# Optimization experiments

Measured on AMD Instinct MI355X. Metric: run time of the kernel, lower is better.

Reference implementation:

```python
import jax, jax.numpy as jnp
import numpy as np

ALPHA = 0.2  # LeakyReLU negative slope
NEG_INF = -9e15


def setup_inputs() -> dict:
    key = jax.random.key(0)
    k1, k2, k3, k4 = jax.random.split(key, 4)
    B, N, Fin, Fout = 8, 2048, 512, 256
    x = jax.random.normal(k1, (B, N, Fin), dtype=jnp.float32)
    adj = jax.random.randint(k2, (B, N, N), 0, 2, dtype=jnp.int32)
    # xavier_uniform-like init, gain=1.414
    limW = 1.414 * np.sqrt(6.0 / (Fin + Fout))
    W = jax.random.uniform(k3, (Fin, Fout), jnp.float32, -limW, limW)
    lima = 1.414 * np.sqrt(6.0 / (2 * Fout + 1))
    a = jax.random.uniform(k4, (2 * Fout, 1), jnp.float32, -lima, lima)
    return {"x": x, "adj": adj, "W": W, "a": a}


def reference(x, adj, W, a):
    # x: [B,N,Fin], adj: [B,N,N], W: [Fin,Fout], a: [2*Fout,1]
    Fout = W.shape[1]
    h = jnp.einsum('bnf,fo->bno', x, W)                      # [B,N,Fout]
    a1 = a[:Fout, 0]                                         # source part
    a2 = a[Fout:, 0]                                         # target part
    # e_ij = LeakyReLU(a1.h_i + a2.h_j) -- decomposed, no O(N^2*2F) tensor
    s = h @ a1                                               # [B,N]
    t = h @ a2                                               # [B,N]
    e = jax.nn.leaky_relu(s[:, :, None] + t[:, None, :], ALPHA)  # [B,N,N]
    e = jnp.where(adj > 0, e, NEG_INF)
    attention = jax.nn.softmax(e, axis=2)                    # dropout p=0 (eval)
    h_prime = jnp.einsum('bij,bjo->bio', attention, h)       # [B,N,Fout]
    return jax.nn.elu(h_prime)                               # concat=True -> ELU
```

## Files before the change

### kernel.cpp

```cpp
#include <hip/hip_runtime.h>
#include <hip/hip_bf16.h>

typedef __attribute__((ext_vector_type(8))) short short8;
typedef __attribute__((ext_vector_type(4))) float f32x4;

constexpr int Bb = 8, NN = 2048, FIN = 512, FOUT = 256;
#define LRALPHA 0.2f
#define MFMA16(a, b, c) __builtin_amdgcn_mfma_f32_16x16x32_bf16((a), (b), (c), 0, 0, 0)

static __device__ __forceinline__ ushort f2bf(float f) {
    unsigned u = __float_as_uint(f);
    u += 0x7fffu + ((u >> 16) & 1u);
    return (ushort)(u >> 16);
}
static __device__ __forceinline__ float bf2f(ushort b) { return __uint_as_float(((unsigned)b) << 16); }

#define LDSBAR() do { asm volatile("s_waitcnt lgkmcnt(0)" ::: "memory"); \
                      __builtin_amdgcn_s_barrier(); \
                      asm volatile("" ::: "memory"); } while (0)
#define BARONLY() do { asm volatile("" ::: "memory"); \
                       __builtin_amdgcn_s_barrier(); \
                       asm volatile("" ::: "memory"); } while (0)

__global__ __launch_bounds__(256) void prep(const float* __restrict__ W,
                                            const float* __restrict__ a,
                                            ushort* __restrict__ WTh,
                                            ushort* __restrict__ WTl,
                                            float* __restrict__ wa1,
                                            float* __restrict__ wa2) {
    __shared__ float r1[4], r2[4];
    const int k = blockIdx.x, n = threadIdx.x;
    const int lane = n & 63, wv = n >> 6;
    const float w = W[(size_t)k * FOUT + n];
    const ushort hi = f2bf(w);
    WTh[(size_t)n * FIN + k] = hi;
    WTl[(size_t)n * FIN + k] = f2bf(w - bf2f(hi));
    float p1 = w * a[n], p2 = w * a[FOUT + n];
#pragma unroll
    for (int m = 1; m < 64; m <<= 1) {
        p1 += __shfl_xor(p1, m);
        p2 += __shfl_xor(p2, m);
    }
    if (lane == 0) { r1[wv] = p1; r2[wv] = p2; }
    __syncthreads();
    if (n == 0) {
        wa1[k] = r1[0] + r1[1] + r1[2] + r1[3];
        wa2[k] = r2[0] + r2[1] + r2[2] + r2[3];
    }
}

__global__ __launch_bounds__(512, 2) void gemm_h(const float* __restrict__ x,
                                                 const ushort* __restrict__ WTh,
                                                 const ushort* __restrict__ WTl,
                                                 const float* __restrict__ wa1,
                                                 const float* __restrict__ wa2,
                                                 ushort* __restrict__ hTh,
                                                 float* __restrict__ sv,
                                                 float* __restrict__ tv) {
    __shared__ ushort Ah[4][2][512];
    __shared__ ushort Tr[8][16][72];

    const int t = threadIdx.x, lane = t & 63, w = t >> 6;
    const int m0 = blockIdx.x * 64;

    const int lr = t >> 3, c8 = (t & 7) * 8;
    const int aif = lr >> 4, akstep = c8 >> 5, ak8 = (c8 >> 3) & 3;
    ushort* adst = &Ah[aif][akstep][(((ak8 << 4) | (lr & 15))) * 8];
    const float* xp = x + (size_t)(m0 + lr) * FIN + c8;

    const size_t b0 = (size_t)(w * 32 + (lane & 15)) * FIN + (lane >> 4) * 8;
    const size_t b1 = b0 + (size_t)16 * FIN;
    const ushort *ph0 = WTh + b0, *pl0 = WTl + b0;
    const ushort *ph1 = WTh + b1, *pl1 = WTl + b1;

    f32x4 acc[4][2];
#pragma unroll
    for (int f = 0; f < 4; ++f) {
        acc[f][0] = (f32x4){0.f, 0.f, 0.f, 0.f};
        acc[f][1] = (f32x4){0.f, 0.f, 0.f, 0.f};
    }
    float sp = 0.f, tp = 0.f;

    float4 xa0 = *(const float4*)(xp + 0),  xa1 = *(const float4*)(xp + 4);
    float4 xb0 = *(const float4*)(xp + 64), xb1 = *(const float4*)(xp + 68);
    float4 xc0, xc1, xd0, xd1;
    short8 A00 = *(const short8*)(ph0 + 0),  A01 = *(const short8*)(pl0 + 0);
    short8 A02 = *(const short8*)(ph0 + 32), A03 = *(const short8*)(pl0 + 32);
    short8 A10 = *(const short8*)(ph1 + 0),  A11 = *(const short8*)(pl1 + 0);
    short8 A12 = *(const short8*)(ph1 + 32), A13 = *(const short8*)(pl1 + 32);
    short8 B00, B01, B02, B03, B10, B11, B12, B13;

    auto phase = [&](int kt, const float4& c0, const float4& c1, float4& nx0, float4& nx1,
                     const short8& g00, const short8& g01, const short8& g02, const short8& g03,
                     const short8& g10, const short8& g11, const short8& g12, const short8& g13,
                     short8& n00, short8& n01, short8& n02, short8& n03,
                     short8& n10, short8& n11, short8& n12, short8& n13) {
        const int k0 = kt * 64;
        const float fv[8] = {c0.x, c0.y, c0.z, c0.w, c1.x, c1.y, c1.z, c1.w};
        short8 vh;
#pragma unroll
        for (int e = 0; e < 8; ++e) vh[e] = (short)f2bf(fv[e]);
        const float4 w1a = *(const float4*)(wa1 + k0 + c8);
        const float4 w1b = *(const float4*)(wa1 + k0 + c8 + 4);
        const float4 w2a = *(const float4*)(wa2 + k0 + c8);
        const float4 w2b = *(const float4*)(wa2 + k0 + c8 + 4);
        sp += fv[0]*w1a.x + fv[1]*w1a.y + fv[2]*w1a.z + fv[3]*w1a.w
            + fv[4]*w1b.x + fv[5]*w1b.y + fv[6]*w1b.z + fv[7]*w1b.w;
        tp += fv[0]*w2a.x + fv[1]*w2a.y + fv[2]*w2a.z + fv[3]*w2a.w
            + fv[4]*w2b.x + fv[5]*w2b.y + fv[6]*w2b.z + fv[7]*w2b.w;
        BARONLY();
        *(short8*)adst = vh;
        LDSBAR();
        const int kx = (kt + 2 < 8 ? kt + 2 : 7) * 64;
        nx0 = *(const float4*)(xp + kx);
        nx1 = *(const float4*)(xp + kx + 4);
        const int kb = (kt + 1 < 8 ? kt + 1 : 7) * 64;
        n00 = *(const short8*)(ph0 + kb);      n01 = *(const short8*)(pl0 + kb);
        n02 = *(const short8*)(ph0 + kb + 32); n03 = *(const short8*)(pl0 + kb + 32);
        n10 = *(const short8*)(ph1 + kb);      n11 = *(const short8*)(pl1 + kb);
        n12 = *(const short8*)(ph1 + kb + 32); n13 = *(const short8*)(pl1 + kb + 32);
#pragma unroll
        for (int f = 0; f < 4; ++f) {
            const short8 a0 = *(const short8*)&Ah[f][0][lane * 8];
            const short8 a1 = *(const short8*)&Ah[f][1][lane * 8];
            acc[f][0] = MFMA16(a0, g00, acc[f][0]);
            acc[f][0] = MFMA16(a0, g01, acc[f][0]);
            acc[f][0] = MFMA16(a1, g02, acc[f][0]);
            acc[f][0] = MFMA16(a1, g03, acc[f][0]);
            acc[f][1] = MFMA16(a0, g10, acc[f][1]);
            acc[f][1] = MFMA16(a0, g11, acc[f][1]);
            acc[f][1] = MFMA16(a1, g12, acc[f][1]);
            acc[f][1] = MFMA16(a1, g13, acc[f][1]);
        }
    };

    for (int kt = 0; kt < 8; kt += 4) {
        phase(kt + 0, xa0, xa1, xc0, xc1, A00,A01,A02,A03,A10,A11,A12,A13,
                                           B00,B01,B02,B03,B10,B11,B12,B13);
        phase(kt + 1, xb0, xb1, xd0, xd1, B00,B01,B02,B03,B10,B11,B12,B13,
                                           A00,A01,A02,A03,A10,A11,A12,A13);
        phase(kt + 2, xc0, xc1, xa0, xa1, A00,A01,A02,A03,A10,A11,A12,A13,
                                           B00,B01,B02,B03,B10,B11,B12,B13);
        phase(kt + 3, xd0, xd1, xb0, xb1, B00,B01,B02,B03,B10,B11,B12,B13,
                                           A00,A01,A02,A03,A10,A11,A12,A13);
    }

    sp += __shfl_xor(sp, 1, 8); sp += __shfl_xor(sp, 2, 8); sp += __shfl_xor(sp, 4, 8);
    tp += __shfl_xor(tp, 1, 8); tp += __shfl_xor(tp, 2, 8); tp += __shfl_xor(tp, 4, 8);
    if ((t & 7) == 0) {
        sv[m0 + lr] = sp;
        tv[m0 + lr] = tp;
    }

    const int rb = (lane >> 4) * 4;
    const int c = lane >> 2, rowb = (lane & 3) * 16;
#pragma unroll
    for (int p = 0; p < 2; ++p) {
        __syncthreads();
#pragma unroll
        for (int f = 0; f < 4; ++f)
#pragma unroll
            for (int r = 0; r < 4; ++r)
                Tr[w][lane & 15][f * 16 + rb + r] = f2bf(acc[f][p][r]);
        __syncthreads();
        const ushort* src = &Tr[w][c][rowb];
        const short8 v0 = *(const short8*)src;
        const short8 v1 = *(const short8*)(src + 8);
        ushort* dst = hTh + ((size_t)(m0 >> 11) * FOUT + w * 32 + p * 16 + c) * NN
                      + (m0 & 2047) + rowb;
        *(short8*)dst = v0;
        *(short8*)(dst + 8) = v1;
    }
}

__global__ __launch_bounds__(512, 2) void gat_fused(const int* __restrict__ adj,
                                                    const ushort* __restrict__ hTh,
                                                    const float* __restrict__ sv,
                                                    const float* __restrict__ tv,
                                                    float* __restrict__ out) {
    __shared__ float t_l[NN];
    __shared__ ushort Pf[2][4][2][512];
    __shared__ float den_l[64];

    const int t = threadIdx.x, lane = t & 63, w = t >> 6;
    const int b = blockIdx.x & 7, i0 = (blockIdx.x >> 3) * 64;

    *(float4*)&t_l[t * 4] = *(const float4*)&tv[b * NN + t * 4];

    const int r = t >> 3, jn = (t & 7) * 8;
    const float s_i = sv[b * NN + i0 + r];
    const int* adjp = adj + ((size_t)b * NN + i0 + r) * NN + jn;
    const int pif = r >> 4, pkstep = jn >> 5, pk8 = (jn >> 3) & 3;
    ushort* pdst0 = &Pf[0][pif][pkstep][((pk8 << 4) | (r & 15)) * 8];
    ushort* pdst1 = &Pf[1][pif][pkstep][((pk8 << 4) | (r & 15)) * 8];

    const ushort* hb = hTh + (size_t)b * FOUT * NN;
    const ushort* h00 = hb + (size_t)(2 * w * 16 + (lane & 15)) * NN + (lane >> 4) * 8;
    const ushort* h10 = hb + (size_t)((2 * w + 1) * 16 + (lane & 15)) * NN + (lane >> 4) * 8;

    f32x4 acc[4][2];
#pragma unroll
    for (int f = 0; f < 4; ++f) {
        acc[f][0] = (f32x4){0.f, 0.f, 0.f, 0.f};
        acc[f][1] = (f32x4){0.f, 0.f, 0.f, 0.f};
    }
    float den_part = 0.f;

    int4 ajA0 = *(const int4*)(adjp +   0), ajA1 = *(const int4*)(adjp +   4);
    int4 ajB0 = *(const int4*)(adjp +  64), ajB1 = *(const int4*)(adjp +  68);
    int4 ajC0 = *(const int4*)(adjp + 128), ajC1 = *(const int4*)(adjp + 132);
    int4 ajD0 = *(const int4*)(adjp + 192), ajD1 = *(const int4*)(adjp + 196);
    short8 X00 = *(const short8*)h00,        X01 = *(const short8*)(h00 + 32);
    short8 X10 = *(const short8*)h10,        X11 = *(const short8*)(h10 + 32);
    short8 Y00 = *(const short8*)(h00 + 64), Y01 = *(const short8*)(h00 + 96);
    short8 Y10 = *(const short8*)(h10 + 64), Y11 = *(const short8*)(h10 + 96);

    __syncthreads();

    auto phase = [&](int jt, ushort* pdst, int rbuf,
                     int4& as0, int4& as1,
                     short8& H00, short8& H01, short8& H10, short8& H11) {
        const int j0 = jt * 64;
        const int avs[8] = {as0.x, as0.y, as0.z, as0.w, as1.x, as1.y, as1.z, as1.w};
        const int jA = min(j0 + 256, NN - 64);
        as0 = *(const int4*)(adjp + jA);
        as1 = *(const int4*)(adjp + jA + 4);
        const float4 tq0 = *(const float4*)&t_l[j0 + jn];
        const float4 tq1 = *(const float4*)&t_l[j0 + jn + 4];
        const float tvv[8] = {tq0.x, tq0.y, tq0.z, tq0.w, tq1.x, tq1.y, tq1.z, tq1.w};
        short8 pv;
#pragma unroll
        for (int e = 0; e < 8; ++e) {
            float v = s_i + tvv[e];
            v = v > 0.f ? v : LRALPHA * v;
            const float wv = avs[e] > 0 ? __expf(v) : 0.f;
            const ushort hbv = f2bf(wv);
            den_part += bf2f(hbv);
            pv[e] = (short)hbv;
        }
        *(short8*)pdst = pv;
        LDSBAR();
        const ushort* pr = &Pf[rbuf][0][0][0] + lane * 8;
        __builtin_amdgcn_s_setprio(1);
#pragma unroll
        for (int f = 0; f < 4; ++f) {
            const short8 a0 = *(const short8*)(pr + f * 1024);
            const short8 a1 = *(const short8*)(pr + f * 1024 + 512);
            acc[f][0] = MFMA16(a0, H00, acc[f][0]);
            acc[f][0] = MFMA16(a1, H01, acc[f][0]);
            acc[f][1] = MFMA16(a0, H10, acc[f][1]);
            acc[f][1] = MFMA16(a1, H11, acc[f][1]);
        }
        __builtin_amdgcn_s_setprio(0);
        const int jH = min(j0 + 128, NN - 64);
        H00 = *(const short8*)(h00 + jH);
        H01 = *(const short8*)(h00 + jH + 32);
        H10 = *(const short8*)(h10 + jH);
        H11 = *(const short8*)(h10 + jH + 32);
    };

    for (int tt = 0; tt < NN / 64; tt += 4) {
        phase(tt + 0, pdst0, 0, ajA0, ajA1, X00, X01, X10, X11);
        phase(tt + 1, pdst1, 1, ajB0, ajB1, Y00, Y01, Y10, Y11);
        phase(tt + 2, pdst0, 0, ajC0, ajC1, X00, X01, X10, X11);
        phase(tt + 3, pdst1, 1, ajD0, ajD1, Y00, Y01, Y10, Y11);
    }

    den_part += __shfl_xor(den_part, 1, 8);
    den_part += __shfl_xor(den_part, 2, 8);
    den_part += __shfl_xor(den_part, 4, 8);
    if ((t & 7) == 0) den_l[r] = den_part;
    __syncthreads();

    const int rb = (lane >> 4) * 4;
#pragma unroll
    for (int f = 0; f < 4; ++f) {
#pragma unroll
        for (int rr = 0; rr < 4; ++rr) {
            const int row = f * 16 + rb + rr;
            const float inv = 1.0f / den_l[row];
#pragma unroll
            for (int cf = 0; cf < 2; ++cf) {
                float v = acc[f][cf][rr] * inv;
                v = v > 0.f ? v : expm1f(v);
                out[((size_t)b * NN + i0 + row) * FOUT + w * 32 + cf * 16 + (lane & 15)] = v;
            }
        }
    }
}

extern "C" void kernel_launch(void* const* d_in, const int* in_sizes, int n_in,
                              void* d_out, int out_size, void* d_ws, size_t ws_size,
                              hipStream_t stream) {
    const float* x   = (const float*)d_in[0];
    const int*   adj = (const int*)d_in[1];
    const float* W   = (const float*)d_in[2];
    const float* a   = (const float*)d_in[3];
    float* out = (float*)d_out;

    ushort* hTh = (ushort*)d_ws;
    float*  sv  = (float*)(hTh + (size_t)Bb * FOUT * NN);
    float*  tv  = sv + Bb * NN;
    ushort* WTh = (ushort*)(tv + Bb * NN);
    ushort* WTl = WTh + (size_t)FIN * FOUT;
    float*  wa1 = (float*)(WTl + (size_t)FIN * FOUT);
    float*  wa2 = wa1 + FIN;

    prep<<<FIN, 256, 0, stream>>>(W, a, WTh, WTl, wa1, wa2);
    gemm_h<<<256, 512, 0, stream>>>(x, WTh, WTl, wa1, wa2, hTh, sv, tv);
    gat_fused<<<256, 512, 0, stream>>>(adj, hTh, sv, tv, out);
}
```

Measured before the change: 261.9 us.

## Fuse prep, GEMM and attention into one cooperative kernel with grid syncs

```diff
diff --git a/kernel.cpp b/kernel.cpp
--- a/kernel.cpp
+++ b/kernel.cpp
@@ -1,5 +1,6 @@
 #include <hip/hip_runtime.h>
 #include <hip/hip_bf16.h>
+#include <hip/hip_cooperative_groups.h>
 
 typedef __attribute__((ext_vector_type(8))) short short8;
 typedef __attribute__((ext_vector_type(4))) float f32x4;
@@ -22,50 +23,51 @@
                        __builtin_amdgcn_s_barrier(); \
                        asm volatile("" ::: "memory"); } while (0)
 
-__global__ __launch_bounds__(256) void prep(const float* __restrict__ W,
-                                            const float* __restrict__ a,
-                                            ushort* __restrict__ WTh,
-                                            ushort* __restrict__ WTl,
-                                            float* __restrict__ wa1,
-                                            float* __restrict__ wa2) {
-    __shared__ float r1[4], r2[4];
-    const int k = blockIdx.x, n = threadIdx.x;
-    const int lane = n & 63, wv = n >> 6;
-    const float w = W[(size_t)k * FOUT + n];
-    const ushort hi = f2bf(w);
-    WTh[(size_t)n * FIN + k] = hi;
-    WTl[(size_t)n * FIN + k] = f2bf(w - bf2f(hi));
-    float p1 = w * a[n], p2 = w * a[FOUT + n];
+struct SPrep { float r1[2][4]; float r2[2][4]; };
+struct SGemm { ushort Ah[4][2][512]; ushort Tr[8][16][72]; };
+struct SGat  { float t_l[NN]; ushort Pf[2][4][2][512]; float den_l[64]; };
+
+static __device__ void prep_body(int bid, int t, SPrep& s,
+                                 const float* __restrict__ W, const float* __restrict__ a,
+                                 ushort* __restrict__ WTh, ushort* __restrict__ WTl,
+                                 float* __restrict__ wa1, float* __restrict__ wa2) {
+    const int half = t >> 8, n = t & 255, lane = t & 63, w4 = (t >> 6) & 3;
+    const int k = bid * 2 + half;
+    const float wv = W[(size_t)k * FOUT + n];
+    float p1 = wv * a[n], p2 = wv * a[FOUT + n];
 #pragma unroll
     for (int m = 1; m < 64; m <<= 1) {
         p1 += __shfl_xor(p1, m);
         p2 += __shfl_xor(p2, m);
     }
-    if (lane == 0) { r1[wv] = p1; r2[wv] = p2; }
+    if (lane == 0) { s.r1[half][w4] = p1; s.r2[half][w4] = p2; }
+    if (t < 256) {
+        const float w0 = W[(size_t)(2 * t) * FOUT + bid];
+        const float w1 = W[(size_t)(2 * t + 1) * FOUT + bid];
+        const ushort h0 = f2bf(w0), h1 = f2bf(w1);
+        const ushort l0 = f2bf(w0 - bf2f(h0)), l1 = f2bf(w1 - bf2f(h1));
+        *(unsigned int*)(WTh + (size_t)bid * FIN + 2 * t) = (unsigned int)h0 | ((unsigned int)h1 << 16);
+        *(unsigned int*)(WTl + (size_t)bid * FIN + 2 * t) = (unsigned int)l0 | ((unsigned int)l1 << 16);
+    }
     __syncthreads();
     if (n == 0) {
-        wa1[k] = r1[0] + r1[1] + r1[2] + r1[3];
-        wa2[k] = r2[0] + r2[1] + r2[2] + r2[3];
-    }
-}
-
-__global__ __launch_bounds__(512, 2) void gemm_h(const float* __restrict__ x,
-                                                 const ushort* __restrict__ WTh,
-                                                 const ushort* __restrict__ WTl,
-                                                 const float* __restrict__ wa1,
-                                                 const float* __restrict__ wa2,
-                                                 ushort* __restrict__ hTh,
-                                                 float* __restrict__ sv,
-                                                 float* __restrict__ tv) {
-    __shared__ ushort Ah[4][2][512];
-    __shared__ ushort Tr[8][16][72];
-
-    const int t = threadIdx.x, lane = t & 63, w = t >> 6;
-    const int m0 = blockIdx.x * 64;
+        wa1[k] = s.r1[half][0] + s.r1[half][1] + s.r1[half][2] + s.r1[half][3];
+        wa2[k] = s.r2[half][0] + s.r2[half][1] + s.r2[half][2] + s.r2[half][3];
+    }
+}
+
+static __device__ void gemm_body(int bid, int t, SGemm& s,
+                                 const float* __restrict__ x,
+                                 const ushort* __restrict__ WTh, const ushort* __restrict__ WTl,
+                                 const float* __restrict__ wa1, const float* __restrict__ wa2,
+                                 ushort* __restrict__ hTh,
+                                 float* __restrict__ sv, float* __restrict__ tv) {
+    const int lane = t & 63, w = t >> 6;
+    const int m0 = bid * 64;
 
     const int lr = t >> 3, c8 = (t & 7) * 8;
     const int aif = lr >> 4, akstep = c8 >> 5, ak8 = (c8 >> 3) & 3;
-    ushort* adst = &Ah[aif][akstep][(((ak8 << 4) | (lr & 15))) * 8];
+    ushort* adst = &s.Ah[aif][akstep][(((ak8 << 4) | (lr & 15))) * 8];
     const float* xp = x + (size_t)(m0 + lr) * FIN + c8;
 
     const size_t b0 = (size_t)(w * 32 + (lane & 15)) * FIN + (lane >> 4) * 8;
@@ -121,8 +123,8 @@
         n12 = *(const short8*)(ph1 + kb + 32); n13 = *(const short8*)(pl1 + kb + 32);
 #pragma unroll
         for (int f = 0; f < 4; ++f) {
-            const short8 a0 = *(const short8*)&Ah[f][0][lane * 8];
-            const short8 a1 = *(const short8*)&Ah[f][1][lane * 8];
+            const short8 a0 = *(const short8*)&s.Ah[f][0][lane * 8];
+            const short8 a1 = *(const short8*)&s.Ah[f][1][lane * 8];
             acc[f][0] = MFMA16(a0, g00, acc[f][0]);
             acc[f][0] = MFMA16(a0, g01, acc[f][0]);
             acc[f][0] = MFMA16(a1, g02, acc[f][0]);
@@ -161,9 +163,9 @@
         for (int f = 0; f < 4; ++f)
 #pragma unroll
             for (int r = 0; r < 4; ++r)
-                Tr[w][lane & 15][f * 16 + rb + r] = f2bf(acc[f][p][r]);
+                s.Tr[w][lane & 15][f * 16 + rb + r] = f2bf(acc[f][p][r]);
         __syncthreads();
-        const ushort* src = &Tr[w][c][rowb];
+        const ushort* src = &s.Tr[w][c][rowb];
         const short8 v0 = *(const short8*)src;
         const short8 v1 = *(const short8*)(src + 8);
         ushort* dst = hTh + ((size_t)(m0 >> 11) * FOUT + w * 32 + p * 16 + c) * NN
@@ -173,26 +175,22 @@
     }
 }
 
-__global__ __launch_bounds__(512, 2) void gat_fused(const int* __restrict__ adj,
-                                                    const ushort* __restrict__ hTh,
-                                                    const float* __restrict__ sv,
-                                                    const float* __restrict__ tv,
-                                                    float* __restrict__ out) {
-    __shared__ float t_l[NN];
-    __shared__ ushort Pf[2][4][2][512];
-    __shared__ float den_l[64];
-
-    const int t = threadIdx.x, lane = t & 63, w = t >> 6;
-    const int b = blockIdx.x & 7, i0 = (blockIdx.x >> 3) * 64;
-
-    *(float4*)&t_l[t * 4] = *(const float4*)&tv[b * NN + t * 4];
+static __device__ void gat_body(int bid, int t, SGat& s,
+                                const int* __restrict__ adj,
+                                const ushort* __restrict__ hTh,
+                                const float* __restrict__ sv, const float* __restrict__ tv,
+                                float* __restrict__ out) {
+    const int lane = t & 63, w = t >> 6;
+    const int b = bid & 7, i0 = (bid >> 3) * 64;
+
+    *(float4*)&s.t_l[t * 4] = *(const float4*)&tv[b * NN + t * 4];
 
     const int r = t >> 3, jn = (t & 7) * 8;
     const float s_i = sv[b * NN + i0 + r];
     const int* adjp = adj + ((size_t)b * NN + i0 + r) * NN + jn;
     const int pif = r >> 4, pkstep = jn >> 5, pk8 = (jn >> 3) & 3;
-    ushort* pdst0 = &Pf[0][pif][pkstep][((pk8 << 4) | (r & 15)) * 8];
-    ushort* pdst1 = &Pf[1][pif][pkstep][((pk8 << 4) | (r & 15)) * 8];
+    ushort* pdst0 = &s.Pf[0][pif][pkstep][((pk8 << 4) | (r & 15)) * 8];
+    ushort* pdst1 = &s.Pf[1][pif][pkstep][((pk8 << 4) | (r & 15)) * 8];
 
     const ushort* hb = hTh + (size_t)b * FOUT * NN;
     const ushort* h00 = hb + (size_t)(2 * w * 16 + (lane & 15)) * NN + (lane >> 4) * 8;
@@ -225,8 +223,8 @@
         const int jA = min(j0 + 256, NN - 64);
         as0 = *(const int4*)(adjp + jA);
         as1 = *(const int4*)(adjp + jA + 4);
-        const float4 tq0 = *(const float4*)&t_l[j0 + jn];
-        const float4 tq1 = *(const float4*)&t_l[j0 + jn + 4];
+        const float4 tq0 = *(const float4*)&s.t_l[j0 + jn];
+        const float4 tq1 = *(const float4*)&s.t_l[j0 + jn + 4];
         const float tvv[8] = {tq0.x, tq0.y, tq0.z, tq0.w, tq1.x, tq1.y, tq1.z, tq1.w};
         short8 pv;
 #pragma unroll
@@ -240,7 +238,7 @@
         }
         *(short8*)pdst = pv;
         LDSBAR();
-        const ushort* pr = &Pf[rbuf][0][0][0] + lane * 8;
+        const ushort* pr = &s.Pf[rbuf][0][0][0] + lane * 8;
         __builtin_amdgcn_s_setprio(1);
 #pragma unroll
         for (int f = 0; f < 4; ++f) {
@@ -269,7 +267,7 @@
     den_part += __shfl_xor(den_part, 1, 8);
     den_part += __shfl_xor(den_part, 2, 8);
     den_part += __shfl_xor(den_part, 4, 8);
-    if ((t & 7) == 0) den_l[r] = den_part;
+    if ((t & 7) == 0) s.den_l[r] = den_part;
     __syncthreads();
 
     const int rb = (lane >> 4) * 4;
@@ -278,7 +276,7 @@
 #pragma unroll
         for (int rr = 0; rr < 4; ++rr) {
             const int row = f * 16 + rb + rr;
-            const float inv = 1.0f / den_l[row];
+            const float inv = 1.0f / s.den_l[row];
 #pragma unroll
             for (int cf = 0; cf < 2; ++cf) {
                 float v = acc[f][cf][rr] * inv;
@@ -287,6 +285,45 @@
             }
         }
     }
+}
+
+union SMU { SPrep p; SGemm g; SGat q; };
+
+__global__ __launch_bounds__(512, 2) void gat_mono(const float* x, const int* adj,
+                                                   const float* W, const float* a,
+                                                   ushort* WTh, ushort* WTl,
+                                                   float* wa1, float* wa2,
+                                                   ushort* hTh, float* sv, float* tv,
+                                                   float* out) {
+    __shared__ SMU sm;
+    const int bid = blockIdx.x, t = threadIdx.x;
+    prep_body(bid, t, sm.p, W, a, WTh, WTl, wa1, wa2);
+    __threadfence();
+    cooperative_groups::this_grid().sync();
+    gemm_body(bid, t, sm.g, x, WTh, WTl, wa1, wa2, hTh, sv, tv);
+    __threadfence();
+    cooperative_groups::this_grid().sync();
+    gat_body(bid, t, sm.q, adj, hTh, sv, tv, out);
+}
+
+__global__ __launch_bounds__(512, 2) void k_prep(const float* W, const float* a,
+                                                 ushort* WTh, ushort* WTl,
+                                                 float* wa1, float* wa2) {
+    __shared__ SPrep s;
+    prep_body(blockIdx.x, threadIdx.x, s, W, a, WTh, WTl, wa1, wa2);
+}
+__global__ __launch_bounds__(512, 2) void k_gemm(const float* x, const ushort* WTh,
+                                                 const ushort* WTl, const float* wa1,
+                                                 const float* wa2, ushort* hTh,
+                                                 float* sv, float* tv) {
+    __shared__ SGemm s;
+    gemm_body(blockIdx.x, threadIdx.x, s, x, WTh, WTl, wa1, wa2, hTh, sv, tv);
+}
+__global__ __launch_bounds__(512, 2) void k_gat(const int* adj, const ushort* hTh,
+                                                const float* sv, const float* tv,
+                                                float* out) {
+    __shared__ SGat s;
+    gat_body(blockIdx.x, threadIdx.x, s, adj, hTh, sv, tv, out);
 }
 
 extern "C" void kernel_launch(void* const* d_in, const int* in_sizes, int n_in,
@@ -306,7 +343,14 @@
     float*  wa1 = (float*)(WTl + (size_t)FIN * FOUT);
     float*  wa2 = wa1 + FIN;
 
-    prep<<<FIN, 256, 0, stream>>>(W, a, WTh, WTl, wa1, wa2);
-    gemm_h<<<256, 512, 0, stream>>>(x, WTh, WTl, wa1, wa2, hTh, sv, tv);
-    gat_fused<<<256, 512, 0, stream>>>(adj, hTh, sv, tv, out);
-}
+    void* args[] = {(void*)&x, (void*)&adj, (void*)&W, (void*)&a,
+                    (void*)&WTh, (void*)&WTl, (void*)&wa1, (void*)&wa2,
+                    (void*)&hTh, (void*)&sv, (void*)&tv, (void*)&out};
+    hipError_t e = hipLaunchCooperativeKernel(reinterpret_cast<const void*>(&gat_mono),
+                                              dim3(256), dim3(512), args, 0u, stream);
+    if (e != hipSuccess) {
+        k_prep<<<256, 512, 0, stream>>>(W, a, WTh, WTl, wa1, wa2);
+        k_gemm<<<256, 512, 0, stream>>>(x, WTh, WTl, wa1, wa2, hTh, sv, tv);
+        k_gat<<<256, 512, 0, stream>>>(adj, hTh, sv, tv, out);
+    }
+}
```

New measurement: 459.9 us. 1.76x slower.
